# Kernel optimization log

Hardware: AMD Instinct MI355X
Metric: run time of the kernel (lower is better)

The kernel has to match this reference:

```python
import jax, jax.numpy as jnp
import numpy as np

K = 256            # number of learned permutations (config['k'])
N = 256            # nb_experts
NOISE_FACTOR = 0.01
TAU_INITIAL = 1e-3
TAU_FINAL = 1e-7
N_ITERS_MIN, N_ITERS_MAX = 20, 150
ITERS_TOTAL = 100 * 1000   # epochs_for_learning_permutation * steps_per_epoch
EPS = 1e-20


def setup_inputs() -> dict:
    key = jax.random.key(0)
    k1, k2 = jax.random.split(key)
    # keras RandomUniform initializer default range is [-0.05, 0.05]
    plw = jax.random.uniform(k1, (K, N, N), jnp.float32, minval=-0.05, maxval=0.05)
    u = jax.random.uniform(k2, (K, N, N), jnp.float32)
    return {"permutation_log_weights": plw, "u": u, "iterations": 5000}


def reference(permutation_log_weights, u, iterations):
    # Linear-in-log10 interpolation of tau and linear interpolation of n_iters
    # over the learning schedule (tfp.math.interp_regular_1d_grid with clamping).
    frac = min(max(float(iterations) / ITERS_TOTAL, 0.0), 1.0)
    log_tau = np.log10(TAU_INITIAL) + frac * (np.log10(TAU_FINAL) - np.log10(TAU_INITIAL))
    tau = np.float32(10.0 ** log_tau)
    n_iters = int(N_ITERS_MIN + frac * (N_ITERS_MAX - N_ITERS_MIN))

    # Gumbel noise from uniform samples, scaled, then temperature scaling.
    noise = -jnp.log(-jnp.log(u + EPS) + EPS) * jnp.float32(NOISE_FACTOR)
    log_alpha = (permutation_log_weights + noise) / tau  # [K, N, N]

    # Log-domain Sinkhorn: alternate row / column log-normalization.
    def step(la, _):
        la = la - jax.scipy.special.logsumexp(la, axis=2, keepdims=True)
        la = la - jax.scipy.special.logsumexp(la, axis=1, keepdims=True)
        return la, None

    log_alpha, _ = jax.lax.scan(step, log_alpha, None, length=n_iters)
    return jnp.exp(log_alpha)  # [K, N, N] near-doubly-stochastic
```

## Files before the change

kernel.cpp:

```cpp
#include <hip/hip_runtime.h>


#define KMAT 256
#define RS2 132
#define RSF 264

typedef float f2 __attribute__((ext_vector_type(2)));
typedef unsigned uint2_ev __attribute__((ext_vector_type(2)));

__device__ __forceinline__ float fast_exp2(float x) {
#if __has_builtin(__builtin_amdgcn_exp2f)
  return __builtin_amdgcn_exp2f(x);
#else
  return exp2f(x);
#endif
}

__device__ __forceinline__ float fast_log2(float x) {
#if __has_builtin(__builtin_amdgcn_logf)
  return __builtin_amdgcn_logf(x);
#else
  return __log2f(x);
#endif
}

__device__ __forceinline__ float fast_rcp(float x) {
#if __has_builtin(__builtin_amdgcn_rcpf)
  return __builtin_amdgcn_rcpf(x);
#else
  return 1.0f / x;
#endif
}

__device__ __forceinline__ f2 f2fma(f2 a, f2 b, f2 c) {
#if __has_builtin(__builtin_elementwise_fma)
  return __builtin_elementwise_fma(a, b, c);
#else
  f2 r; r[0] = fmaf(a[0], b[0], c[0]); r[1] = fmaf(a[1], b[1], c[1]); return r;
#endif
}

template <int CTRL>
__device__ __forceinline__ float dpp_movf(float x) {
  return __int_as_float(
      __builtin_amdgcn_update_dpp(0, __float_as_int(x), CTRL, 0xf, 0xf, true));
}

__device__ __forceinline__ uint2_ev pl16_swap(unsigned a, unsigned b) {
  return __builtin_amdgcn_permlane16_swap(a, b, false, false);
}

__device__ __forceinline__ float hgroup_max(float x) {
  x = fmaxf(x, dpp_movf<0x121>(x));
  x = fmaxf(x, dpp_movf<0x122>(x));
  x = fmaxf(x, dpp_movf<0x124>(x));
  x = fmaxf(x, dpp_movf<0x128>(x));
  uint2_ev r = pl16_swap(__float_as_uint(x), __float_as_uint(x));
  return fmaxf(__uint_as_float(r[0]), __uint_as_float(r[1]));
}

__device__ __forceinline__ float hgroup_sum(float x) {
  x += dpp_movf<0x121>(x);
  x += dpp_movf<0x122>(x);
  x += dpp_movf<0x124>(x);
  x += dpp_movf<0x128>(x);
  uint2_ev r = pl16_swap(__float_as_uint(x), __float_as_uint(x));
  return __uint_as_float(r[0]) + __uint_as_float(r[1]);
}

__device__ __forceinline__ float gumbel_la(float p, float uv, float scale) {
  float lnu = fast_log2(uv + 1e-20f) * 0.69314718056f;
  float g = fast_log2(1e-20f - lnu) * (-0.0069314718056f);
  return (p + g) * scale;
}

__global__ __launch_bounds__(1024)
__attribute__((amdgpu_waves_per_eu(4, 4)))
void lp_sinkhorn_kernel(
    const float* __restrict__ plw, const float* __restrict__ uin,
    const int* __restrict__ itp, float* __restrict__ out) {
  const int k = blockIdx.x;
  const int t = threadIdx.x;
  const int br = t >> 5;
  const int bc = t & 31;
  const int wv = t >> 6;
  const int lane = t & 63;

  __shared__ f2 red2[32][RS2];
  __shared__ f2 colvp[128];
  float* redF = (float*)red2;
  float* colv = (float*)colvp;

  const int slot = 16 * wv + (lane >> 2);
  const int q = lane & 3;

  double frac = (double)itp[0] * 1e-5;
  frac = frac < 0.0 ? 0.0 : (frac > 1.0 ? 1.0 : frac);
  const int n_iters = (int)(20.0 + frac * 130.0);
  const float tauf = (float)exp2((-3.0 - 4.0 * frac) * 3.3219280948873623);
  const float scale = (float)(1.4426950408889634 / (double)tauf);

  f2 la[8][4];

  const float4* p4 = (const float4*)plw + k * 16384;
  const float4* u4 = (const float4*)uin + k * 16384;
#pragma unroll
  for (int i = 0; i < 8; ++i) {
    const int ridx = ((br << 3) + i) * 64 + (bc << 1);
    float4 p0 = p4[ridx];
    float4 p1 = p4[ridx + 1];
    float4 v0 = u4[ridx];
    float4 v1 = u4[ridx + 1];
    la[i][0] = f2{gumbel_la(p0.x, v0.x, scale), gumbel_la(p0.y, v0.y, scale)};
    la[i][1] = f2{gumbel_la(p0.z, v0.z, scale), gumbel_la(p0.w, v0.w, scale)};
    la[i][2] = f2{gumbel_la(p1.x, v1.x, scale), gumbel_la(p1.y, v1.y, scale)};
    la[i][3] = f2{gumbel_la(p1.z, v1.z, scale), gumbel_la(p1.w, v1.w, scale)};
  }

#pragma unroll
  for (int i = 0; i < 8; ++i) {
    float m = fmaxf(la[i][0][0], la[i][0][1]);
#pragma unroll
    for (int p = 1; p < 4; ++p) m = fmaxf(m, fmaxf(la[i][p][0], la[i][p][1]));
    m = hgroup_max(m);
    float s = 0.f;
#pragma unroll
    for (int p = 0; p < 4; ++p)
      s += fast_exp2(la[i][p][0] - m) + fast_exp2(la[i][p][1] - m);
    s = hgroup_sum(s);
    const float lse = m + fast_log2(s);
#pragma unroll
    for (int p = 0; p < 4; ++p) la[i][p] -= f2{lse, lse};
  }

  {
#pragma unroll
    for (int p = 0; p < 4; ++p) {
      f2 m = la[0][p];
#pragma unroll
      for (int i = 1; i < 8; ++i)
        m = f2{fmaxf(m[0], la[i][p][0]), fmaxf(m[1], la[i][p][1])};
      red2[br][32 * p + bc] = m;
    }
    __syncthreads();

    {
      float v = redF[q * RSF + slot];
#pragma unroll
      for (int m = 1; m < 8; ++m)
        v = fmaxf(v, redF[(q + 4 * m) * RSF + slot]);
      v = fmaxf(v, dpp_movf<0xB1>(v));
      v = fmaxf(v, dpp_movf<0x4E>(v));
      if (q == 0) colv[slot] = v;
    }
    __syncthreads();

#pragma unroll
    for (int p = 0; p < 4; ++p) {
      const f2 mj = colvp[32 * p + bc];
      f2 s = f2{0.f, 0.f};
#pragma unroll
      for (int i = 0; i < 8; ++i)
        s = f2{s[0] + fast_exp2(la[i][p][0] - mj[0]),
               s[1] + fast_exp2(la[i][p][1] - mj[1])};
      red2[br][32 * p + bc] = s;
    }
    __syncthreads();

    {
      float v = redF[q * RSF + slot];
#pragma unroll
      for (int m = 1; m < 8; ++m) v += redF[(q + 4 * m) * RSF + slot];
      v += dpp_movf<0xB1>(v);
      v += dpp_movf<0x4E>(v);
      const float lse = colv[slot] + fast_log2(v);
      if (q == 0) colv[slot] = lse;
    }
    __syncthreads();

#pragma unroll
    for (int p = 0; p < 4; ++p) {
      const f2 lse = colvp[32 * p + bc];
#pragma unroll
      for (int i = 0; i < 8; ++i)
        la[i][p] = f2{fast_exp2(la[i][p][0] - lse[0]),
                      fast_exp2(la[i][p][1] - lse[1])};
    }
  }

  float u[8] = {1.f, 1.f, 1.f, 1.f, 1.f, 1.f, 1.f, 1.f};
  f2 v2[4] = {f2{1.f, 1.f}, f2{1.f, 1.f}, f2{1.f, 1.f}, f2{1.f, 1.f}};

  for (int iter = 1; iter < n_iters; ++iter) {
#pragma unroll
    for (int i = 0; i < 8; ++i) {
      f2 a01 = la[i][0] * v2[0];
      a01 = f2fma(la[i][1], v2[1], a01);
      f2 a23 = la[i][2] * v2[2];
      a23 = f2fma(la[i][3], v2[3], a23);
      f2 acc = a01 + a23;
      u[i] = fast_rcp(hgroup_sum(acc[0] + acc[1]));
    }

    f2 cs[4];
    {
      const f2 ub0 = f2{u[0], u[0]};
#pragma unroll
      for (int p = 0; p < 4; ++p) cs[p] = la[0][p] * ub0;
    }
#pragma unroll
    for (int i = 1; i < 8; ++i) {
      const f2 ub = f2{u[i], u[i]};
#pragma unroll
      for (int p = 0; p < 4; ++p) cs[p] = f2fma(la[i][p], ub, cs[p]);
    }
#pragma unroll
    for (int p = 0; p < 4; ++p) red2[br][32 * p + bc] = cs[p];
    __syncthreads();

    {
      float v = redF[q * RSF + slot];
#pragma unroll
      for (int m = 1; m < 8; ++m) v += redF[(q + 4 * m) * RSF + slot];
      v += dpp_movf<0xB1>(v);
      v += dpp_movf<0x4E>(v);
      if (q == 0) colv[slot] = fast_rcp(v);
    }
    __syncthreads();

#pragma unroll
    for (int p = 0; p < 4; ++p) v2[p] = colvp[32 * p + bc];
  }

  float4* o4 = (float4*)out + k * 16384;
#pragma unroll
  for (int i = 0; i < 8; ++i) {
    const int ridx = ((br << 3) + i) * 64 + (bc << 1);
    const f2 ub = f2{u[i], u[i]};
    f2 r0 = (la[i][0] * ub) * v2[0];
    f2 r1 = (la[i][1] * ub) * v2[1];
    f2 r2 = (la[i][2] * ub) * v2[2];
    f2 r3 = (la[i][3] * ub) * v2[3];
    float4 a, b;
    a.x = r0[0]; a.y = r0[1]; a.z = r1[0]; a.w = r1[1];
    b.x = r2[0]; b.y = r2[1]; b.z = r3[0]; b.w = r3[1];
    o4[ridx] = a;
    o4[ridx + 1] = b;
  }
}

extern "C" void kernel_launch(void* const* d_in, const int* in_sizes, int n_in,
                              void* d_out, int out_size, void* d_ws,
                              size_t ws_size, hipStream_t stream) {
  const float* plw = (const float*)d_in[0];
  const float* u = (const float*)d_in[1];
  const int* iters = (const int*)d_in[2];
  float* out = (float*)d_out;
  (void)in_sizes; (void)n_in; (void)out_size; (void)d_ws; (void)ws_size;
  lp_sinkhorn_kernel<<<dim3(KMAT), dim3(1024), 0, stream>>>(plw, u, iters, out);
}
```

Measured before the change: 86.25 us.

## Use LDS atomic column sums with triple-buffered accumulators, one barrier per iteration

Replaces the two-phase shared-memory column reduction (write partials, barrier, cross-lane reduce, barrier) with float atomicAdd into a 128-entry LDS column-sum buffer. Three buffers rotate so that zeroing the next accumulator and reading the previous one need only a single __syncthreads per Sinkhorn iteration. The initial log-domain column normalization is also replaced by a linear-domain first iteration: row softmax via exp and reciprocal, then column sums through the same atomic path. The cost is 32-way LDS atomic contention per column address, and floating-point atomic ordering is nondeterministic.

```diff
diff --git a/kernel.cpp b/kernel.cpp
--- a/kernel.cpp
+++ b/kernel.cpp
@@ -2,8 +2,6 @@
 
 
 #define KMAT 256
-#define RS2 132
-#define RSF 264
 
 typedef float f2 __attribute__((ext_vector_type(2)));
 typedef unsigned uint2_ev __attribute__((ext_vector_type(2)));
@@ -83,16 +81,10 @@
   const int t = threadIdx.x;
   const int br = t >> 5;
   const int bc = t & 31;
-  const int wv = t >> 6;
-  const int lane = t & 63;
-
-  __shared__ f2 red2[32][RS2];
-  __shared__ f2 colvp[128];
-  float* redF = (float*)red2;
-  float* colv = (float*)colvp;
-
-  const int slot = 16 * wv + (lane >> 2);
-  const int q = lane & 3;
+
+  __shared__ f2 cbuf[3][128];
+
+  if (t < 128) cbuf[1][t] = f2{0.f, 0.f};
 
   double frac = (double)itp[0] * 1e-5;
   frac = frac < 0.0 ? 0.0 : (frac > 1.0 ? 1.0 : frac);
@@ -125,73 +117,49 @@
     m = hgroup_max(m);
     float s = 0.f;
 #pragma unroll
-    for (int p = 0; p < 4; ++p)
-      s += fast_exp2(la[i][p][0] - m) + fast_exp2(la[i][p][1] - m);
+    for (int p = 0; p < 4; ++p) {
+      la[i][p] = f2{fast_exp2(la[i][p][0] - m), fast_exp2(la[i][p][1] - m)};
+      s += la[i][p][0] + la[i][p][1];
+    }
     s = hgroup_sum(s);
-    const float lse = m + fast_log2(s);
-#pragma unroll
-    for (int p = 0; p < 4; ++p) la[i][p] -= f2{lse, lse};
-  }
+    const float r = fast_rcp(s);
+#pragma unroll
+    for (int p = 0; p < 4; ++p) la[i][p] *= f2{r, r};
+  }
+
+  __syncthreads();
+
+  f2* Ca = cbuf[1];
+  f2* Cr = cbuf[0];
+  f2* Cz = cbuf[2];
+  float u[8] = {1.f, 1.f, 1.f, 1.f, 1.f, 1.f, 1.f, 1.f};
 
   {
-#pragma unroll
-    for (int p = 0; p < 4; ++p) {
-      f2 m = la[0][p];
-#pragma unroll
-      for (int i = 1; i < 8; ++i)
-        m = f2{fmaxf(m[0], la[i][p][0]), fmaxf(m[1], la[i][p][1])};
-      red2[br][32 * p + bc] = m;
-    }
+    f2 cs[4];
+#pragma unroll
+    for (int p = 0; p < 4; ++p) cs[p] = la[0][p];
+#pragma unroll
+    for (int i = 1; i < 8; ++i)
+#pragma unroll
+      for (int p = 0; p < 4; ++p) cs[p] += la[i][p];
+    float* CaF = (float*)Ca;
+#pragma unroll
+    for (int p = 0; p < 4; ++p) {
+      atomicAdd(&CaF[64 * p + 2 * bc], cs[p][0]);
+      atomicAdd(&CaF[64 * p + 2 * bc + 1], cs[p][1]);
+    }
+    if (t < 128) Cz[t] = f2{0.f, 0.f};
     __syncthreads();
-
-    {
-      float v = redF[q * RSF + slot];
-#pragma unroll
-      for (int m = 1; m < 8; ++m)
-        v = fmaxf(v, redF[(q + 4 * m) * RSF + slot]);
-      v = fmaxf(v, dpp_movf<0xB1>(v));
-      v = fmaxf(v, dpp_movf<0x4E>(v));
-      if (q == 0) colv[slot] = v;
-    }
-    __syncthreads();
-
-#pragma unroll
-    for (int p = 0; p < 4; ++p) {
-      const f2 mj = colvp[32 * p + bc];
-      f2 s = f2{0.f, 0.f};
-#pragma unroll
-      for (int i = 0; i < 8; ++i)
-        s = f2{s[0] + fast_exp2(la[i][p][0] - mj[0]),
-               s[1] + fast_exp2(la[i][p][1] - mj[1])};
-      red2[br][32 * p + bc] = s;
-    }
-    __syncthreads();
-
-    {
-      float v = redF[q * RSF + slot];
-#pragma unroll
-      for (int m = 1; m < 8; ++m) v += redF[(q + 4 * m) * RSF + slot];
-      v += dpp_movf<0xB1>(v);
-      v += dpp_movf<0x4E>(v);
-      const float lse = colv[slot] + fast_log2(v);
-      if (q == 0) colv[slot] = lse;
-    }
-    __syncthreads();
-
-#pragma unroll
-    for (int p = 0; p < 4; ++p) {
-      const f2 lse = colvp[32 * p + bc];
-#pragma unroll
-      for (int i = 0; i < 8; ++i)
-        la[i][p] = f2{fast_exp2(la[i][p][0] - lse[0]),
-                      fast_exp2(la[i][p][1] - lse[1])};
-    }
-  }
-
-  float u[8] = {1.f, 1.f, 1.f, 1.f, 1.f, 1.f, 1.f, 1.f};
-  f2 v2[4] = {f2{1.f, 1.f}, f2{1.f, 1.f}, f2{1.f, 1.f}, f2{1.f, 1.f}};
-
-  for (int iter = 1; iter < n_iters; ++iter) {
+    f2* tmp = Ca; Ca = Cz; Cz = Cr; Cr = tmp;
+  }
+
+  for (int it = 2; it <= n_iters; ++it) {
+    f2 v2[4];
+#pragma unroll
+    for (int p = 0; p < 4; ++p) {
+      const f2 c = Cr[32 * p + bc];
+      v2[p] = f2{fast_rcp(c[0]), fast_rcp(c[1])};
+    }
 #pragma unroll
     for (int i = 0; i < 8; ++i) {
       f2 a01 = la[i][0] * v2[0];
@@ -201,7 +169,6 @@
       f2 acc = a01 + a23;
       u[i] = fast_rcp(hgroup_sum(acc[0] + acc[1]));
     }
-
     f2 cs[4];
     {
       const f2 ub0 = f2{u[0], u[0]};
@@ -214,24 +181,23 @@
 #pragma unroll
       for (int p = 0; p < 4; ++p) cs[p] = f2fma(la[i][p], ub, cs[p]);
     }
-#pragma unroll
-    for (int p = 0; p < 4; ++p) red2[br][32 * p + bc] = cs[p];
+    float* CaF = (float*)Ca;
+#pragma unroll
+    for (int p = 0; p < 4; ++p) {
+      atomicAdd(&CaF[64 * p + 2 * bc], cs[p][0]);
+      atomicAdd(&CaF[64 * p + 2 * bc + 1], cs[p][1]);
+    }
+    if (t < 128) Cz[t] = f2{0.f, 0.f};
     __syncthreads();
-
-    {
-      float v = redF[q * RSF + slot];
-#pragma unroll
-      for (int m = 1; m < 8; ++m) v += redF[(q + 4 * m) * RSF + slot];
-      v += dpp_movf<0xB1>(v);
-      v += dpp_movf<0x4E>(v);
-      if (q == 0) colv[slot] = fast_rcp(v);
-    }
-    __syncthreads();
-
-#pragma unroll
-    for (int p = 0; p < 4; ++p) v2[p] = colvp[32 * p + bc];
-  }
-
+    f2* tmp = Ca; Ca = Cz; Cz = Cr; Cr = tmp;
+  }
+
+  f2 v2[4];
+#pragma unroll
+  for (int p = 0; p < 4; ++p) {
+    const f2 c = Cr[32 * p + bc];
+    v2[p] = f2{fast_rcp(c[0]), fast_rcp(c[1])};
+  }
   float4* o4 = (float4*)out + k * 16384;
 #pragma unroll
   for (int i = 0; i < 8; ++i) {
```

Measured after the change: 322.0 us. 3.73x slower.
